# Kernel tuning notes

Measured on AMD Instinct MI355X. Metric: run time of the kernel, lower is better.

The kernel has to match this reference:

```python
import jax, jax.numpy as jnp
import numpy as np

DIM_EMB = 1024
NUM_HEADS = 16
DIM_HEAD = DIM_EMB // NUM_HEADS  # 64


def setup_inputs() -> dict:
    key = jax.random.key(0)
    k1, k2, k3 = jax.random.split(key, 3)
    x = jax.random.normal(k1, (4, 2048, DIM_EMB), dtype=jnp.float32)
    # nn.Linear(dim_embedding, 3*h*d, bias=False): weight shape [out, in]
    w_qkv = jax.random.normal(k2, (3 * NUM_HEADS * DIM_HEAD, DIM_EMB), dtype=jnp.float32) * (DIM_EMB ** -0.5)
    w_out = jax.random.normal(k3, (DIM_EMB, NUM_HEADS * DIM_HEAD), dtype=jnp.float32) * ((NUM_HEADS * DIM_HEAD) ** -0.5)
    return {"x": x, "w_qkv": w_qkv, "w_out": w_out}


def reference(x, w_qkv, w_out):
    b, t, _ = x.shape
    scale = DIM_HEAD ** -0.5
    qkv = jnp.einsum('bte,fe->btf', x, w_qkv)  # [b, t, 3*h*d]
    qkv = qkv.reshape(b, t, 3, NUM_HEADS, DIM_HEAD)  # fused dim order (k h d)
    q, k, v = qkv[:, :, 0], qkv[:, :, 1], qkv[:, :, 2]  # each [b, t, h, d]
    scores = jnp.einsum('bihd,bjhd->bhij', q, k) * scale  # [b, h, t, t]
    weights = jax.nn.softmax(scores, axis=-1)
    attn = jnp.einsum('bhij,bjhd->bhid', weights, v)  # [b, h, t, d]
    concat = attn.transpose(0, 2, 1, 3).reshape(b, t, NUM_HEADS * DIM_HEAD)
    return jnp.einsum('btf,ef->bte', concat, w_out)
```

## Files before the change

### kernel.cpp

```cpp
#include <hip/hip_runtime.h>

#define DI __device__ __forceinline__

typedef float  f32x2  __attribute__((ext_vector_type(2)));
typedef float  f32x4  __attribute__((ext_vector_type(4)));
typedef float  f32x16 __attribute__((ext_vector_type(16)));
typedef __bf16 bf16x8 __attribute__((ext_vector_type(8)));
typedef unsigned u32x2 __attribute__((ext_vector_type(2)));
typedef unsigned u32x4 __attribute__((ext_vector_type(4)));

static constexpr int TB   = 2048;
static constexpr int NTOK = 8192;
static constexpr int EMB  = 1024;
static constexpr int FQKV = 3072;

DI unsigned short f2bf(float f) {
  union { float f; unsigned u; } v; v.f = f;
  unsigned r = v.u + 0x7FFFu + ((v.u >> 16) & 1u);
  return (unsigned short)(r >> 16);
}

DI unsigned pack2bf(float a, float b) {
#if __has_builtin(__builtin_amdgcn_cvt_pk_bf16_f32)
  typedef __bf16 bf16x2 __attribute__((ext_vector_type(2)));
  bf16x2 r = __builtin_amdgcn_cvt_pk_bf16_f32(a, b);
  return __builtin_bit_cast(unsigned, r);
#else
  unsigned ua = __builtin_bit_cast(unsigned, a) + 0x8000u;
  unsigned ub = __builtin_bit_cast(unsigned, b) + 0x8000u;
  return __builtin_amdgcn_perm(ub, ua, 0x07060302u);
#endif
}

DI void plswap(unsigned& a, unsigned& b) {
#if __has_builtin(__builtin_amdgcn_permlane32_swap)
  u32x2 r = __builtin_amdgcn_permlane32_swap(a, b, false, false);
  a = r.x; b = r.y;
#else
  const bool hi = (threadIdx.x & 32) != 0;
  unsigned ax = (unsigned)__shfl_xor((int)a, 32);
  unsigned bx = (unsigned)__shfl_xor((int)b, 32);
  unsigned na = hi ? bx : a;
  unsigned nb = hi ? b : ax;
  a = na; b = nb;
#endif
}

DI bf16x8 frag4(unsigned a, unsigned b, unsigned c, unsigned d) {
  u32x4 u = {a, b, c, d};
  return __builtin_bit_cast(bf16x8, u);
}

DI void gload16(const void* g, void* l) {
  __builtin_amdgcn_global_load_lds(
      (__attribute__((address_space(1))) void*)(g),
      (__attribute__((address_space(3))) void*)(l), 16, 0, 0);
}

DI void syncdrain() {
  __builtin_amdgcn_s_waitcnt(0);
  __syncthreads();
}

__global__ __launch_bounds__(256)
void cvt_kernel(const float4* __restrict__ x, const float4* __restrict__ wq,
                const float4* __restrict__ wo,
                ushort4* __restrict__ xb, ushort4* __restrict__ wqb,
                ushort4* __restrict__ wob) {
  const int i  = blockIdx.x * 256 + threadIdx.x;
  const int nx = NTOK * EMB / 4;
  const int nq = FQKV * EMB / 4;
  float4 v; ushort4* dst;
  if (i < nx)           { v = x[i];           dst = xb  + i; }
  else if (i < nx + nq) { v = wq[i - nx];     dst = wqb + (i - nx); }
  else                  { v = wo[i - nx - nq]; dst = wob + (i - nx - nq); }
  ushort4 p;
  p.x = f2bf(v.x); p.y = f2bf(v.y); p.z = f2bf(v.z); p.w = f2bf(v.w);
  *dst = p;
}

template <int MODE>
__global__ __launch_bounds__(256)
void gemm_bt(const unsigned short* __restrict__ A,
             const unsigned short* __restrict__ Bt,
             const int K,
             unsigned short* __restrict__ qk,
             unsigned short* __restrict__ vT,
             float* __restrict__ outp) {
  __shared__ unsigned short sA[128 * 32];
  __shared__ unsigned short sB[128 * 32];
  const int tid  = threadIdx.x;
  const int w    = tid >> 6;
  const int l    = tid & 63;
  const int quad = l >> 4;
  const int lr   = l & 15;
  const int n0   = blockIdx.x * 128;
  const int m0   = blockIdx.y * 128;
  const int wm   = (w >> 1) * 64;
  const int wn   = (w & 1) * 64;

  f32x4 acc[4][4];
#pragma unroll
  for (int i = 0; i < 4; ++i)
#pragma unroll
    for (int j = 0; j < 4; ++j) acc[i][j] = {0.f, 0.f, 0.f, 0.f};

  const int srow = l >> 2;
  const int sg   = (l & 3) ^ ((l >> 3) & 3);
  const unsigned short* gA = A  + (long)(m0 + w * 32 + srow) * K + sg * 8;
  const unsigned short* gB = Bt + (long)(n0 + w * 32 + srow) * K + sg * 8;
  unsigned short* lA = sA + w * 1024;
  unsigned short* lB = sB + w * 1024;
  const int swz = (lr >> 1) & 3;

  for (int k0 = 0; k0 < K; k0 += 32) {
    gload16(gA + k0,          lA);
    gload16(gA + k0 + 16 * K, lA + 512);
    gload16(gB + k0,          lB);
    gload16(gB + k0 + 16 * K, lB + 512);
    syncdrain();
    bf16x8 af[4], bfr[4];
#pragma unroll
    for (int rt = 0; rt < 4; ++rt)
      af[rt] = *(const bf16x8*)(sA + (wm + rt * 16 + lr) * 32 + (quad ^ swz) * 8);
#pragma unroll
    for (int ct = 0; ct < 4; ++ct)
      bfr[ct] = *(const bf16x8*)(sB + (wn + ct * 16 + lr) * 32 + (quad ^ swz) * 8);
#pragma unroll
    for (int rt = 0; rt < 4; ++rt)
#pragma unroll
      for (int ct = 0; ct < 4; ++ct)
        acc[rt][ct] = __builtin_amdgcn_mfma_f32_16x16x32_bf16(af[rt], bfr[ct],
                                                              acc[rt][ct], 0, 0, 0);
    __syncthreads();
  }

  if (MODE == 0) {
    if (n0 < 2048) {
      const float qs = (n0 < 1024) ? 0.18033688011112042f : 1.0f;
#pragma unroll
      for (int rt = 0; rt < 4; ++rt) {
        const int row = m0 + wm + rt * 16 + quad * 4;
#pragma unroll
        for (int ct = 0; ct < 4; ++ct) {
          const int col = n0 + wn + ct * 16 + lr;
#pragma unroll
          for (int r = 0; r < 4; ++r)
            qk[(long)(row + r) * 2048 + col] = f2bf(acc[rt][ct][r] * qs);
        }
      }
    } else {
#pragma unroll
      for (int rt = 0; rt < 4; ++rt) {
        const int tok = m0 + wm + rt * 16 + quad * 4;
        const int bb  = tok >> 11, tt = tok & 2047;
#pragma unroll
        for (int ct = 0; ct < 4; ++ct) {
          const int fv = n0 - 2048 + wn + ct * 16 + lr;
          ushort4 p;
          p.x = f2bf(acc[rt][ct][0]); p.y = f2bf(acc[rt][ct][1]);
          p.z = f2bf(acc[rt][ct][2]); p.w = f2bf(acc[rt][ct][3]);
          *(ushort4*)(vT + ((long)(bb * 1024 + fv)) * 2048 + tt) = p;
        }
      }
    }
  } else {
#pragma unroll
    for (int rt = 0; rt < 4; ++rt) {
      const int row = m0 + wm + rt * 16 + quad * 4;
#pragma unroll
      for (int ct = 0; ct < 4; ++ct) {
        const int col = n0 + wn + ct * 16 + lr;
#pragma unroll
        for (int r = 0; r < 4; ++r)
          outp[(long)(row + r) * 1024 + col] = acc[rt][ct][r];
      }
    }
  }
}

__global__ __launch_bounds__(256)
void attn_kernel(const unsigned short* __restrict__ qk,
                 const unsigned short* __restrict__ vT,
                 unsigned short* __restrict__ attnb) {
  __shared__ unsigned short sK[2][64 * 64];
  __shared__ unsigned short sV[2][64 * 64];
  const int tid = threadIdx.x;
  const int w   = tid >> 6;
  const int l   = tid & 63;
  const int l31 = l & 31;
  const int lh  = l >> 5;
  const int h8  = lh * 8;
  const int bh  = blockIdx.x;
  const int hh  = bh & 15;
  const long tokbase = (long)(bh >> 4) * TB;
  const int qbase = blockIdx.y * 256 + w * 64;

  bf16x8 qf[2][4];
#pragma unroll
  for (int qs = 0; qs < 2; ++qs) {
    const unsigned short* qptr =
        qk + (tokbase + qbase + qs * 32 + l31) * 2048 + hh * 64 + h8;
#pragma unroll
    for (int s = 0; s < 4; ++s) qf[qs][s] = *(const bf16x8*)(qptr + s * 16);
  }

  const int srow = l >> 3;
  const int g    = (l & 7) ^ srow;
  const unsigned short* kbase =
      qk + (tokbase + w * 16 + srow) * 2048 + 1024 + hh * 64 + g * 8;
  const unsigned short* vbase =
      vT + ((long)bh * 64 + w * 16 + srow) * 2048 + g * 8;

  f32x16 oacc[2][2] = {{{}, {}}, {{}, {}}};
  f32x2 lp2[2] = {{0.f, 0.f}, {0.f, 0.f}};

  gload16(kbase,            &sK[0][(w * 16 + 0) * 64]);
  gload16(kbase + 8 * 2048, &sK[0][(w * 16 + 8) * 64]);
  gload16(vbase,            &sV[0][(w * 16 + 0) * 64]);
  gload16(vbase + 8 * 2048, &sV[0][(w * 16 + 8) * 64]);
  syncdrain();

  for (int t = 0; t < 32; ++t) {
    const int buf = t & 1;
    if (t + 1 < 32) {
      const int k0 = (t + 1) * 64;
      const int nb = buf ^ 1;
      gload16(kbase + (long)k0 * 2048,            &sK[nb][(w * 16 + 0) * 64]);
      gload16(kbase + (long)k0 * 2048 + 8 * 2048, &sK[nb][(w * 16 + 8) * 64]);
      gload16(vbase + k0,                         &sV[nb][(w * 16 + 0) * 64]);
      gload16(vbase + k0 + 8 * 2048,              &sV[nb][(w * 16 + 8) * 64]);
    }
    const unsigned short* bK = sK[buf];
    const unsigned short* bV = sV[buf];

#pragma unroll
    for (int G = 0; G < 2; ++G) {
      f32x16 sacc[2] = {{}, {}};
#pragma unroll
      for (int s = 0; s < 4; ++s) {
        const int key = G * 32 + l31;
        const int p   = (s * 2 + lh) ^ (key & 7);
        const bf16x8 kf = *(const bf16x8*)(bK + key * 64 + p * 8);
        sacc[0] = __builtin_amdgcn_mfma_f32_32x32x16_bf16(kf, qf[0][s], sacc[0], 0, 0, 0);
        sacc[1] = __builtin_amdgcn_mfma_f32_32x32x16_bf16(kf, qf[1][s], sacc[1], 0, 0, 0);
      }
      bf16x8 pp[2][2];
#pragma unroll
      for (int qs = 0; qs < 2; ++qs) {
        float e[16];
#pragma unroll
        for (int i = 0; i < 16; ++i) e[i] = __builtin_amdgcn_exp2f(sacc[qs][i]);
#pragma unroll
        for (int i = 0; i < 8; ++i) {
          f32x2 pr = {e[2 * i], e[2 * i + 1]};
          lp2[qs] += pr;
        }
        unsigned d[8];
#pragma unroll
        for (int i = 0; i < 8; ++i) d[i] = pack2bf(e[2 * i], e[2 * i + 1]);
        plswap(d[0], d[2]); plswap(d[1], d[3]);
        plswap(d[4], d[6]); plswap(d[5], d[7]);
        pp[qs][0] = frag4(d[0], d[1], d[2], d[3]);
        pp[qs][1] = frag4(d[4], d[5], d[6], d[7]);
      }
#pragma unroll
      for (int sub = 0; sub < 2; ++sub) {
        const int gt  = (G * 2 + sub) * 2 + lh;
        const int d0r = l31, d1r = 32 + l31;
        const bf16x8 vf0 = *(const bf16x8*)(bV + d0r * 64 + ((gt ^ (d0r & 7))) * 8);
        const bf16x8 vf1 = *(const bf16x8*)(bV + d1r * 64 + ((gt ^ (d1r & 7))) * 8);
#pragma unroll
        for (int qs = 0; qs < 2; ++qs) {
          oacc[qs][0] = __builtin_amdgcn_mfma_f32_32x32x16_bf16(pp[qs][sub], vf0, oacc[qs][0], 0, 0, 0);
          oacc[qs][1] = __builtin_amdgcn_mfma_f32_32x32x16_bf16(pp[qs][sub], vf1, oacc[qs][1], 0, 0, 0);
        }
      }
    }
    syncdrain();
  }

#pragma unroll
  for (int qs = 0; qs < 2; ++qs) {
    const float lp = lp2[qs].x + lp2[qs].y;
    const float fs = lp + __shfl_xor(lp, 32);
    const float rc = 1.0f / fs;
#pragma unroll
    for (int r = 0; r < 16; ++r) {
      const int row = (r & 3) + 8 * (r >> 2) + 4 * lh;
      const float sc = __shfl(rc, row);
      const long base = (tokbase + qbase + qs * 32 + row) * 1024 + hh * 64;
      attnb[base + l31]      = f2bf(oacc[qs][0][r] * sc);
      attnb[base + 32 + l31] = f2bf(oacc[qs][1][r] * sc);
    }
  }
}

extern "C" void kernel_launch(void* const* d_in, const int* in_sizes, int n_in,
                              void* d_out, int out_size, void* d_ws, size_t ws_size,
                              hipStream_t stream) {
  const float* x    = (const float*)d_in[0];
  const float* wqkv = (const float*)d_in[1];
  const float* wout = (const float*)d_in[2];
  float* outp = (float*)d_out;

  unsigned short* xb    = (unsigned short*)d_ws;
  unsigned short* wqkvb = xb    + (long)NTOK * EMB;
  unsigned short* woutb = wqkvb + (long)FQKV * EMB;
  unsigned short* qkb   = woutb + (long)EMB * EMB;
  unsigned short* vTb   = qkb   + (long)NTOK * 2048;
  unsigned short* attnb = vTb   + (long)4 * 16 * 64 * TB;

  cvt_kernel<<<12288, 256, 0, stream>>>(
      (const float4*)x, (const float4*)wqkv, (const float4*)wout,
      (ushort4*)xb, (ushort4*)wqkvb, (ushort4*)woutb);

  gemm_bt<0><<<dim3(24, 64), 256, 0, stream>>>(xb, wqkvb, EMB, qkb, vTb, nullptr);

  attn_kernel<<<dim3(64, 8), 256, 0, stream>>>(qkb, vTb, attnb);

  gemm_bt<1><<<dim3(8, 64), 256, 0, stream>>>(attnb, woutb, EMB, nullptr, nullptr, outp);
}
```

Before: 275.9 us.

## Vectorize GEMM epilogue stores, enlarge attention KV tile, compute row sums on MFMA

In the GEMM, the Q/K and output-projection tiles swap MFMA operands so each lane holds four consecutive columns, which lets the epilogue write ushort4/float4 vectors instead of scalar stores. In the attention kernel, the per-iteration K/V tile grows from 64 to 128 keys with a new swizzle, halving the number of loop iterations and barriers. Softmax denominators are now accumulated with MFMAs against a ones vector rather than VALU adds and shuffles. It also sets launch_bounds(256,2) on the attention kernel, and the larger shared-memory tiles may limit occupancy. Summing the bf16-rounded probabilities on the MFMA also changes numerics slightly.

```diff
diff --git a/kernel.cpp b/kernel.cpp
--- a/kernel.cpp
+++ b/kernel.cpp
@@ -98,6 +98,7 @@
   const int m0   = blockIdx.y * 128;
   const int wm   = (w >> 1) * 64;
   const int wn   = (w & 1) * 64;
+  const bool TRANS = (MODE == 1) || (n0 < 2048);
 
   f32x4 acc[4][4];
 #pragma unroll
@@ -126,12 +127,21 @@
 #pragma unroll
     for (int ct = 0; ct < 4; ++ct)
       bfr[ct] = *(const bf16x8*)(sB + (wn + ct * 16 + lr) * 32 + (quad ^ swz) * 8);
-#pragma unroll
-    for (int rt = 0; rt < 4; ++rt)
-#pragma unroll
-      for (int ct = 0; ct < 4; ++ct)
-        acc[rt][ct] = __builtin_amdgcn_mfma_f32_16x16x32_bf16(af[rt], bfr[ct],
-                                                              acc[rt][ct], 0, 0, 0);
+    if (TRANS) {
+#pragma unroll
+      for (int rt = 0; rt < 4; ++rt)
+#pragma unroll
+        for (int ct = 0; ct < 4; ++ct)
+          acc[rt][ct] = __builtin_amdgcn_mfma_f32_16x16x32_bf16(bfr[ct], af[rt],
+                                                                acc[rt][ct], 0, 0, 0);
+    } else {
+#pragma unroll
+      for (int rt = 0; rt < 4; ++rt)
+#pragma unroll
+        for (int ct = 0; ct < 4; ++ct)
+          acc[rt][ct] = __builtin_amdgcn_mfma_f32_16x16x32_bf16(af[rt], bfr[ct],
+                                                                acc[rt][ct], 0, 0, 0);
+    }
     __syncthreads();
   }
 
@@ -140,13 +150,14 @@
       const float qs = (n0 < 1024) ? 0.18033688011112042f : 1.0f;
 #pragma unroll
       for (int rt = 0; rt < 4; ++rt) {
-        const int row = m0 + wm + rt * 16 + quad * 4;
+        const int row = m0 + wm + rt * 16 + lr;
 #pragma unroll
         for (int ct = 0; ct < 4; ++ct) {
-          const int col = n0 + wn + ct * 16 + lr;
-#pragma unroll
-          for (int r = 0; r < 4; ++r)
-            qk[(long)(row + r) * 2048 + col] = f2bf(acc[rt][ct][r] * qs);
+          const int col = n0 + wn + ct * 16 + quad * 4;
+          ushort4 p;
+          p.x = f2bf(acc[rt][ct][0] * qs); p.y = f2bf(acc[rt][ct][1] * qs);
+          p.z = f2bf(acc[rt][ct][2] * qs); p.w = f2bf(acc[rt][ct][3] * qs);
+          *(ushort4*)(qk + (long)row * 2048 + col) = p;
         }
       }
     } else {
@@ -167,24 +178,22 @@
   } else {
 #pragma unroll
     for (int rt = 0; rt < 4; ++rt) {
-      const int row = m0 + wm + rt * 16 + quad * 4;
+      const int row = m0 + wm + rt * 16 + lr;
 #pragma unroll
       for (int ct = 0; ct < 4; ++ct) {
-        const int col = n0 + wn + ct * 16 + lr;
-#pragma unroll
-        for (int r = 0; r < 4; ++r)
-          outp[(long)(row + r) * 1024 + col] = acc[rt][ct][r];
-      }
-    }
-  }
-}
-
-__global__ __launch_bounds__(256)
+        const int col = n0 + wn + ct * 16 + quad * 4;
+        *(f32x4*)(outp + (long)row * 1024 + col) = acc[rt][ct];
+      }
+    }
+  }
+}
+
+__global__ __launch_bounds__(256, 2)
 void attn_kernel(const unsigned short* __restrict__ qk,
                  const unsigned short* __restrict__ vT,
                  unsigned short* __restrict__ attnb) {
-  __shared__ unsigned short sK[2][64 * 64];
-  __shared__ unsigned short sV[2][64 * 64];
+  __shared__ unsigned short sK[2][128 * 64];
+  __shared__ unsigned short sV[2][64 * 128];
   const int tid = threadIdx.x;
   const int w   = tid >> 6;
   const int l   = tid & 63;
@@ -205,37 +214,47 @@
     for (int s = 0; s < 4; ++s) qf[qs][s] = *(const bf16x8*)(qptr + s * 16);
   }
 
-  const int srow = l >> 3;
-  const int g    = (l & 7) ^ srow;
+  const int srow8 = l >> 3;
+  const int g8    = (l & 7) ^ srow8;
   const unsigned short* kbase =
-      qk + (tokbase + w * 16 + srow) * 2048 + 1024 + hh * 64 + g * 8;
-  const unsigned short* vbase =
-      vT + ((long)bh * 64 + w * 16 + srow) * 2048 + g * 8;
+      qk + (tokbase + w * 32 + srow8) * 2048 + 1024 + hh * 64 + g8 * 8;
+  const int srow4 = l >> 4;
+  const unsigned short* vbase_i[4];
+#pragma unroll
+  for (int i = 0; i < 4; ++i) {
+    const int gi = (l & 15) ^ (i * 4 + srow4);
+    vbase_i[i] = vT + ((long)bh * 64 + w * 16 + i * 4 + srow4) * 2048 + gi * 8;
+  }
 
   f32x16 oacc[2][2] = {{{}, {}}, {{}, {}}};
-  f32x2 lp2[2] = {{0.f, 0.f}, {0.f, 0.f}};
-
-  gload16(kbase,            &sK[0][(w * 16 + 0) * 64]);
-  gload16(kbase + 8 * 2048, &sK[0][(w * 16 + 8) * 64]);
-  gload16(vbase,            &sV[0][(w * 16 + 0) * 64]);
-  gload16(vbase + 8 * 2048, &sV[0][(w * 16 + 8) * 64]);
+  f32x16 lacc[2] = {{}, {}};
+  bf16x8 ones;
+#pragma unroll
+  for (int i = 0; i < 8; ++i) ones[i] = (__bf16)1.0f;
+
+#pragma unroll
+  for (int i = 0; i < 4; ++i) {
+    gload16(kbase + (long)(i * 8) * 2048, &sK[0][(w * 32 + i * 8) * 64]);
+    gload16(vbase_i[i],                   &sV[0][(w * 16 + i * 4) * 128]);
+  }
   syncdrain();
 
-  for (int t = 0; t < 32; ++t) {
+  for (int t = 0; t < 16; ++t) {
     const int buf = t & 1;
-    if (t + 1 < 32) {
-      const int k0 = (t + 1) * 64;
+    if (t + 1 < 16) {
+      const int k0 = (t + 1) * 128;
       const int nb = buf ^ 1;
-      gload16(kbase + (long)k0 * 2048,            &sK[nb][(w * 16 + 0) * 64]);
-      gload16(kbase + (long)k0 * 2048 + 8 * 2048, &sK[nb][(w * 16 + 8) * 64]);
-      gload16(vbase + k0,                         &sV[nb][(w * 16 + 0) * 64]);
-      gload16(vbase + k0 + 8 * 2048,              &sV[nb][(w * 16 + 8) * 64]);
+#pragma unroll
+      for (int i = 0; i < 4; ++i) {
+        gload16(kbase + (long)(k0 + i * 8) * 2048, &sK[nb][(w * 32 + i * 8) * 64]);
+        gload16(vbase_i[i] + k0,                   &sV[nb][(w * 16 + i * 4) * 128]);
+      }
     }
     const unsigned short* bK = sK[buf];
     const unsigned short* bV = sV[buf];
 
 #pragma unroll
-    for (int G = 0; G < 2; ++G) {
+    for (int G = 0; G < 4; ++G) {
       f32x16 sacc[2] = {{}, {}};
 #pragma unroll
       for (int s = 0; s < 4; ++s) {
@@ -251,11 +270,6 @@
         float e[16];
 #pragma unroll
         for (int i = 0; i < 16; ++i) e[i] = __builtin_amdgcn_exp2f(sacc[qs][i]);
-#pragma unroll
-        for (int i = 0; i < 8; ++i) {
-          f32x2 pr = {e[2 * i], e[2 * i + 1]};
-          lp2[qs] += pr;
-        }
         unsigned d[8];
 #pragma unroll
         for (int i = 0; i < 8; ++i) d[i] = pack2bf(e[2 * i], e[2 * i + 1]);
@@ -264,12 +278,16 @@
         pp[qs][0] = frag4(d[0], d[1], d[2], d[3]);
         pp[qs][1] = frag4(d[4], d[5], d[6], d[7]);
       }
+      lacc[0] = __builtin_amdgcn_mfma_f32_32x32x16_bf16(pp[0][0], ones, lacc[0], 0, 0, 0);
+      lacc[0] = __builtin_amdgcn_mfma_f32_32x32x16_bf16(pp[0][1], ones, lacc[0], 0, 0, 0);
+      lacc[1] = __builtin_amdgcn_mfma_f32_32x32x16_bf16(pp[1][0], ones, lacc[1], 0, 0, 0);
+      lacc[1] = __builtin_amdgcn_mfma_f32_32x32x16_bf16(pp[1][1], ones, lacc[1], 0, 0, 0);
 #pragma unroll
       for (int sub = 0; sub < 2; ++sub) {
-        const int gt  = (G * 2 + sub) * 2 + lh;
-        const int d0r = l31, d1r = 32 + l31;
-        const bf16x8 vf0 = *(const bf16x8*)(bV + d0r * 64 + ((gt ^ (d0r & 7))) * 8);
-        const bf16x8 vf1 = *(const bf16x8*)(bV + d1r * 64 + ((gt ^ (d1r & 7))) * 8);
+        const int gt = G * 4 + sub * 2 + lh;
+        const int p  = gt ^ (l31 & 15);
+        const bf16x8 vf0 = *(const bf16x8*)(bV + l31 * 128 + p * 8);
+        const bf16x8 vf1 = *(const bf16x8*)(bV + (32 + l31) * 128 + p * 8);
 #pragma unroll
         for (int qs = 0; qs < 2; ++qs) {
           oacc[qs][0] = __builtin_amdgcn_mfma_f32_32x32x16_bf16(pp[qs][sub], vf0, oacc[qs][0], 0, 0, 0);
@@ -282,13 +300,10 @@
 
 #pragma unroll
   for (int qs = 0; qs < 2; ++qs) {
-    const float lp = lp2[qs].x + lp2[qs].y;
-    const float fs = lp + __shfl_xor(lp, 32);
-    const float rc = 1.0f / fs;
 #pragma unroll
     for (int r = 0; r < 16; ++r) {
+      const float sc = 1.0f / lacc[qs][r];
       const int row = (r & 3) + 8 * (r >> 2) + 4 * lh;
-      const float sc = __shfl(rc, row);
       const long base = (tokbase + qbase + qs * 32 + row) * 1024 + hh * 64;
       attnb[base + l31]      = f2bf(oacc[qs][0][r] * sc);
       attnb[base + 32 + l31] = f2bf(oacc[qs][1][r] * sc);
```

Measured after the change: 310.4 us. 12.5% more time.
